# Kernel optimization log

Hardware: AMD Instinct MI355X
Metric: run time of the kernel (lower is better)

The kernel has to match this reference:

```python
import jax, jax.numpy as jnp
import numpy as np

N_NODES = 100000
IN_CH = 128
HID = 64
N_EDGES = 1600000
NEG_SLOPE = 0.2


def setup_inputs() -> dict:
    key = jax.random.key(0)
    k1, k2, k3, k4, k5, k6 = jax.random.split(key, 6)
    x = jax.random.normal(k1, (N_NODES, IN_CH), dtype=jnp.float32)
    edge_index = jax.random.randint(k2, (2, N_EDGES), 0, N_NODES, dtype=jnp.int64)
    # Glorot-style init for GATConv params (heads=1)
    s_w = (2.0 / (IN_CH + HID)) ** 0.5
    W = jax.random.normal(k3, (IN_CH, HID), dtype=jnp.float32) * s_w
    s_a = (2.0 / (1 + HID)) ** 0.5
    att_src = jax.random.normal(k4, (HID,), dtype=jnp.float32) * s_a
    att_dst = jax.random.normal(k5, (HID,), dtype=jnp.float32) * s_a
    bias = jnp.zeros((HID,), dtype=jnp.float32)
    return {"x": x, "edge_index": edge_index, "W": W, "att_src": att_src,
            "att_dst": att_dst, "bias": bias}


def reference(x, edge_index, W, att_src, att_dst, bias):
    N = x.shape[0]
    # PyG GATConv default: add self-loops
    loop = jnp.arange(N, dtype=edge_index.dtype)
    src = jnp.concatenate([edge_index[0], loop])  # message source j
    dst = jnp.concatenate([edge_index[1], loop])  # message target i

    h = x @ W                      # [N, HID]
    a_src = h @ att_src            # [N]
    a_dst = h @ att_dst            # [N]

    # per-edge attention logit: LeakyReLU(a_src[j] + a_dst[i])
    e = jax.nn.leaky_relu(a_src[src] + a_dst[dst], NEG_SLOPE)  # [E+N]
    # numerically-stable segment softmax over destination node
    m = jax.ops.segment_max(e, dst, num_segments=N)
    e = jnp.exp(e - m[dst])
    denom = jax.ops.segment_sum(e, dst, num_segments=N)
    alpha = e / (denom[dst] + 1e-16)               # [E+N]

    # scatter-aggregate weighted source features, then bias
    out = jax.ops.segment_sum(alpha[:, None] * h[src], dst, num_segments=N)
    out = out + bias               # [N, HID]
    return out, alpha[:, None]     # alpha shaped [E+N, heads=1]
```

## Files before the change

kernel.cpp:

```cpp
#include <hip/hip_runtime.h>

#define NN 100000
#define IC 128
#define HD 64
#define NEG 0.2f
#define NPB 64
#define NBKT ((NN + NPB - 1) / NPB)
#define CAP 1536
#define TILE 4096
#define NIT 8

typedef float f32x4 __attribute__((ext_vector_type(4)));
typedef short s16x8 __attribute__((ext_vector_type(8)));

__device__ __forceinline__ unsigned short f32_to_bf16u(float f) {
  union { float f; unsigned int i; } v;
  v.f = f;
  unsigned int b = v.i;
  b += 0x7FFFu + ((b >> 16) & 1u);
  return (unsigned short)(b >> 16);
}

__global__ __launch_bounds__(256) void k_gemm(const float* __restrict__ x,
                                              const float* __restrict__ W,
                                              const float* __restrict__ att_s,
                                              const float* __restrict__ att_d,
                                              unsigned short* __restrict__ hb,
                                              float* __restrict__ as_,
                                              float* __restrict__ ad_,
                                              int* __restrict__ bktcur) {
  __shared__ unsigned short xb[64 * 128];
  __shared__ unsigned short wt[64 * 128];
  const int tid = threadIdx.x;
  const int n0 = blockIdx.x * 64;
  if (tid == 0 && blockIdx.x < NBKT) bktcur[blockIdx.x] = 0;

  #pragma unroll
  for (int i = 0; i < 8; ++i) {
    int f = i * 256 + tid;
    int r = f >> 5, k0 = (f & 31) << 2;
    float4 v = make_float4(0.f, 0.f, 0.f, 0.f);
    if (n0 + r < NN) v = *(const float4*)&x[(size_t)(n0 + r) * IC + k0];
    ushort4 u;
    u.x = f32_to_bf16u(v.x); u.y = f32_to_bf16u(v.y);
    u.z = f32_to_bf16u(v.z); u.w = f32_to_bf16u(v.w);
    int idx = r * 128 + k0;
    *(ushort4*)&xb[idx ^ ((r & 7) << 3)] = u;
  }
  #pragma unroll
  for (int i = 0; i < 8; ++i) {
    int f = i * 256 + tid;
    int k = f >> 4, c0 = (f & 15) << 2;
    float4 v = *(const float4*)&W[k * HD + c0];
    const float* vf = (const float*)&v;
    #pragma unroll
    for (int j = 0; j < 4; ++j) {
      int c = c0 + j;
      int idx = c * 128 + k;
      wt[idx ^ ((c & 7) << 3)] = f32_to_bf16u(vf[j]);
    }
  }
  __syncthreads();

  const int wv = tid >> 6, lane = tid & 63;
  const int fr = lane & 15;
  const int fq = lane >> 4;
  const int nodeR = wv * 16 + fr;
  f32x4 acc[4] = {};
  #pragma unroll
  for (int kb = 0; kb < 4; ++kb) {
    int ks = kb * 32 + fq * 8;
    int ia = nodeR * 128 + ks;
    s16x8 af = *(s16x8*)&xb[ia ^ ((nodeR & 7) << 3)];
    #pragma unroll
    for (int cg = 0; cg < 4; ++cg) {
      int col = cg * 16 + fr;
      int ib = col * 128 + ks;
      s16x8 bfr = *(s16x8*)&wt[ib ^ ((col & 7) << 3)];
      acc[cg] = __builtin_amdgcn_mfma_f32_16x16x32_bf16(af, bfr, acc[cg], 0, 0, 0);
    }
  }

  float atts[4], attd[4];
  #pragma unroll
  for (int cg = 0; cg < 4; ++cg) {
    atts[cg] = att_s[cg * 16 + fr];
    attd[cg] = att_d[cg * 16 + fr];
  }
  __syncthreads();
  unsigned short* ho = xb;

  #pragma unroll
  for (int j = 0; j < 4; ++j) {
    int nrel = wv * 16 + fq * 4 + j;
    float ps = acc[0][j]*atts[0] + acc[1][j]*atts[1]
             + acc[2][j]*atts[2] + acc[3][j]*atts[3];
    float pd = acc[0][j]*attd[0] + acc[1][j]*attd[1]
             + acc[2][j]*attd[2] + acc[3][j]*attd[3];
    #pragma unroll
    for (int mk = 1; mk < 16; mk <<= 1) {
      ps += __shfl_xor(ps, mk);
      pd += __shfl_xor(pd, mk);
    }
    if (fr == 0 && n0 + nrel < NN) { as_[n0 + nrel] = ps; ad_[n0 + nrel] = pd; }
    #pragma unroll
    for (int cg = 0; cg < 4; ++cg)
      ho[nrel * 72 + cg * 16 + fr] = f32_to_bf16u(acc[cg][j]);
  }
  __syncthreads();

  {
    int node = tid >> 2, ch = (tid & 3) << 4;
    if (n0 + node < NN) {
      ushort4 a0 = *(ushort4*)&ho[node * 72 + ch];
      ushort4 a1 = *(ushort4*)&ho[node * 72 + ch + 4];
      ushort4 a2 = *(ushort4*)&ho[node * 72 + ch + 8];
      ushort4 a3 = *(ushort4*)&ho[node * 72 + ch + 12];
      unsigned short* dst = &hb[(size_t)(n0 + node) * HD + ch];
      *(ushort4*)(dst) = a0;
      *(ushort4*)(dst + 4) = a1;
      *(ushort4*)(dst + 8) = a2;
      *(ushort4*)(dst + 12) = a3;
    }
  }
}

__global__ __launch_bounds__(512) void k_part(const int* __restrict__ ei,
                                              const float* __restrict__ as_,
                                              const float* __restrict__ ad_,
                                              int* __restrict__ bktcur,
                                              int2* __restrict__ bktbuf,
                                              float* __restrict__ p_lin,
                                              int E, int M) {
  __shared__ int lcnt[NBKT];
  __shared__ int gbs[NBKT];
  const int tid = threadIdx.x;
  const int base = blockIdx.x * TILE;

  for (int c = tid; c < NBKT; c += 512) lcnt[c] = 0;
  __syncthreads();

  int pkx[NIT], rb[NIT];
  float tv[NIT];
  #pragma unroll
  for (int i = 0; i < NIT; ++i) {
    int m = base + i * 512 + tid;
    if (m < M) {
      int s, d;
      if (m < E) { s = ei[m]; d = ei[E + m]; }
      else       { s = m - E; d = s; }
      int b = d >> 6;
      pkx[i] = (s << 6) | (d & 63);
      tv[i] = as_[s] + ad_[d];
      int r = atomicAdd(&lcnt[b], 1);
      rb[i] = (b << 12) | r;
    } else rb[i] = -1;
  }
  __syncthreads();

  for (int c = tid; c < NBKT; c += 512) {
    int v = lcnt[c];
    gbs[c] = v ? atomicAdd(&bktcur[c], v) : 0;
  }
  __syncthreads();

  #pragma unroll
  for (int i = 0; i < NIT; ++i) {
    if (rb[i] >= 0) {
      int m = base + i * 512 + tid;
      float t = tv[i];
      t = t > 0.f ? t : NEG * t;
      float p = __expf(t);
      p_lin[m] = p;
      int b = (unsigned)rb[i] >> 12, r = rb[i] & 4095;
      int slot = gbs[b] + r;
      if (slot < CAP)
        bktbuf[(size_t)b * CAP + slot] = make_int2(pkx[i], __float_as_int(p));
    }
  }
}

__global__ __launch_bounds__(256) void k_pg(const int* __restrict__ bktcur,
                                            const int2* __restrict__ bktbuf,
                                            const unsigned short* __restrict__ hb,
                                            const float* __restrict__ bias,
                                            float* __restrict__ out,
                                            float* __restrict__ denom) {
  __shared__ int2 sp[CAP];
  __shared__ int cnt2[NPB], nstart[NPB], cur[NPB];
  __shared__ float dls[NPB];
  const int b = blockIdx.x;
  const int d0 = b << 6;
  const int tid = threadIdx.x;
  const int cnt = min(bktcur[b], CAP);
  const int2* mybuf = bktbuf + (size_t)b * CAP;
  const char* hbb = (const char*)hb;

  if (tid < NPB) { cnt2[tid] = 0; dls[tid] = 0.f; }
  __syncthreads();
  for (int e = tid; e < cnt; e += 256) atomicAdd(&cnt2[mybuf[e].x & 63], 1);
  __syncthreads();

  if (tid < 64) {
    int a = cnt2[tid];
    int va = a;
    #pragma unroll
    for (int off = 1; off < 64; off <<= 1) {
      int na = __shfl_up(va, off);
      if (tid >= off) va += na;
    }
    nstart[tid] = va - a;
    cur[tid] = va - a;
  }
  __syncthreads();
  for (int e = tid; e < cnt; e += 256) {
    int2 v = mybuf[e];
    int slot = atomicAdd(&cur[v.x & 63], 1);
    sp[slot] = make_int2((v.x & ~63) << 1, v.y);
  }
  __syncthreads();

  const int wv = tid >> 6, lane = tid & 63;
  const int half = lane >> 5;
  const int hl = lane & 31;
  const unsigned chb = (unsigned)hl << 2;
  const float2 bs2 = *(const float2*)&bias[2 * hl];

  for (int n = wv; n < NPB; n += 4) {
    if (d0 + n >= NN) break;
    int beg = nstart[n], end = beg + cnt2[n];
    float ax = 0.f, ay = 0.f, dens = 0.f;
    int e = beg;
    for (; e + 8 <= end; e += 8) {
      #pragma unroll
      for (int j = 0; j < 4; ++j) {
        int2 v = sp[e + 2 * j + half];
        unsigned u = *(const unsigned*)(hbb + ((unsigned)v.x + chb));
        float p = __int_as_float(v.y);
        dens += p;
        ax += p * __uint_as_float(u << 16);
        ay += p * __uint_as_float(u & 0xffff0000u);
      }
    }
    {
      #pragma unroll
      for (int j = 0; j < 4; ++j) {
        int idx = e + 2 * j + half;
        if (idx < end) {
          int2 v = sp[idx];
          unsigned u = *(const unsigned*)(hbb + ((unsigned)v.x + chb));
          float p = __int_as_float(v.y);
          dens += p;
          ax += p * __uint_as_float(u << 16);
          ay += p * __uint_as_float(u & 0xffff0000u);
        }
      }
    }
    ax += __shfl_xor(ax, 32);
    ay += __shfl_xor(ay, 32);
    dens += __shfl_xor(dens, 32);
    if (half == 0) {
      float rd = 1.f / (dens + 1e-16f);
      float2 o;
      o.x = ax * rd + bs2.x;
      o.y = ay * rd + bs2.y;
      *(float2*)&out[(size_t)(d0 + n) * HD + 2 * hl] = o;
      if (hl == 0) dls[n] = dens;
    }
  }
  __syncthreads();
  if (tid < NPB && d0 + tid < NN) denom[d0 + tid] = dls[tid];
}

__global__ __launch_bounds__(256) void k_alpha(const int* __restrict__ ei,
                                               const float* __restrict__ p_lin,
                                               const float* __restrict__ denom,
                                               float* __restrict__ alpha_out,
                                               int E, int M) {
  int m = blockIdx.x * 256 + threadIdx.x;
  if (m >= M) return;
  int d = (m < E) ? ei[E + m] : (m - E);
  alpha_out[m] = p_lin[m] / (denom[d] + 1e-16f);
}

extern "C" void kernel_launch(void* const* d_in, const int* in_sizes, int n_in,
                              void* d_out, int out_size, void* d_ws, size_t ws_size,
                              hipStream_t stream) {
  const float* x     = (const float*)d_in[0];
  const int*   ei    = (const int*)d_in[1];
  const float* W     = (const float*)d_in[2];
  const float* att_s = (const float*)d_in[3];
  const float* att_d = (const float*)d_in[4];
  const float* bias  = (const float*)d_in[5];

  const int E = in_sizes[1] / 2;
  const int M = E + NN;

  float* out       = (float*)d_out;
  float* alpha_out = out + (size_t)NN * HD;

  char* w = (char*)d_ws;
  auto alloc = [&](size_t bytes) {
    char* p = w;
    w += (bytes + 15) & ~(size_t)15;
    return p;
  };
  unsigned short* hb = (unsigned short*)alloc(sizeof(unsigned short) * (size_t)NN * HD);
  float* as_    = (float*)alloc(sizeof(float) * NN);
  float* ad_    = (float*)alloc(sizeof(float) * NN);
  float* denom  = (float*)alloc(sizeof(float) * NN);
  float* p_lin  = (float*)alloc(sizeof(float) * (size_t)M);
  int*   bktcur = (int*)alloc(sizeof(int) * NBKT);
  int2*  bktbuf = (int2*)alloc(sizeof(int2) * (size_t)NBKT * CAP);

  k_gemm<<<(NN + 63) / 64, 256, 0, stream>>>(x, W, att_s, att_d, hb, as_, ad_,
                                             bktcur);
  k_part<<<(M + TILE - 1) / TILE, 512, 0, stream>>>(ei, as_, ad_, bktcur,
                                                    bktbuf, p_lin, E, M);
  k_pg<<<NBKT, 256, 0, stream>>>(bktcur, bktbuf, hb, bias, out, denom);
  k_alpha<<<(M + 255) / 256, 256, 0, stream>>>(ei, p_lin, denom, alpha_out,
                                               E, M);
}
```

Measured before the change: 105.8 us.

## Split destination-bucket counters into 8 partitions to cut global atomic contention

The partition kernel now writes each edge into one of 8 per-partition bucket arrays (chosen by block index), so global atomicAdds on bucket cursors spread over 8x more counters. The gather kernel loads all partition segments of its bucket into shared memory before the per-node sort, which adds an extra LDS staging pass and doubles shared memory use (two CAP-sized int2 arrays). Per-partition capacity of 256 could overflow for skewed inputs and silently drop edges.

```diff
diff --git a/kernel.cpp b/kernel.cpp
--- a/kernel.cpp
+++ b/kernel.cpp
@@ -7,6 +7,8 @@
 #define NPB 64
 #define NBKT ((NN + NPB - 1) / NPB)
 #define CAP 1536
+#define CAP2 256
+#define NPART 8
 #define TILE 4096
 #define NIT 8
 
@@ -33,7 +35,7 @@
   __shared__ unsigned short wt[64 * 128];
   const int tid = threadIdx.x;
   const int n0 = blockIdx.x * 64;
-  if (tid == 0 && blockIdx.x < NBKT) bktcur[blockIdx.x] = 0;
+  if (tid < NPART && blockIdx.x < NBKT) bktcur[tid * NBKT + blockIdx.x] = 0;
 
   #pragma unroll
   for (int i = 0; i < 8; ++i) {
@@ -136,6 +138,9 @@
   __shared__ int gbs[NBKT];
   const int tid = threadIdx.x;
   const int base = blockIdx.x * TILE;
+  const int part = blockIdx.x & (NPART - 1);
+  int* mycur = bktcur + part * NBKT;
+  int2* mybuf = bktbuf + (size_t)part * NBKT * CAP2;
 
   for (int c = tid; c < NBKT; c += 512) lcnt[c] = 0;
   __syncthreads();
@@ -160,7 +165,7 @@
 
   for (int c = tid; c < NBKT; c += 512) {
     int v = lcnt[c];
-    gbs[c] = v ? atomicAdd(&bktcur[c], v) : 0;
+    gbs[c] = v ? atomicAdd(&mycur[c], v) : 0;
   }
   __syncthreads();
 
@@ -174,8 +179,8 @@
       p_lin[m] = p;
       int b = (unsigned)rb[i] >> 12, r = rb[i] & 4095;
       int slot = gbs[b] + r;
-      if (slot < CAP)
-        bktbuf[(size_t)b * CAP + slot] = make_int2(pkx[i], __float_as_int(p));
+      if (slot < CAP2)
+        mybuf[(size_t)b * CAP2 + slot] = make_int2(pkx[i], __float_as_int(p));
     }
   }
 }
@@ -186,19 +191,36 @@
                                             const float* __restrict__ bias,
                                             float* __restrict__ out,
                                             float* __restrict__ denom) {
+  __shared__ int2 spRaw[CAP];
   __shared__ int2 sp[CAP];
   __shared__ int cnt2[NPB], nstart[NPB], cur[NPB];
   __shared__ float dls[NPB];
+  __shared__ int pcnt[NPART], pbase[NPART];
   const int b = blockIdx.x;
   const int d0 = b << 6;
   const int tid = threadIdx.x;
-  const int cnt = min(bktcur[b], CAP);
-  const int2* mybuf = bktbuf + (size_t)b * CAP;
   const char* hbb = (const char*)hb;
 
   if (tid < NPB) { cnt2[tid] = 0; dls[tid] = 0.f; }
-  __syncthreads();
-  for (int e = tid; e < cnt; e += 256) atomicAdd(&cnt2[mybuf[e].x & 63], 1);
+  if (tid < NPART) pcnt[tid] = min(bktcur[tid * NBKT + b], CAP2);
+  __syncthreads();
+  if (tid == 0) {
+    int s = 0;
+    #pragma unroll
+    for (int p = 0; p < NPART; ++p) { pbase[p] = s; s += pcnt[p]; }
+  }
+  __syncthreads();
+  const int total = min(pbase[NPART - 1] + pcnt[NPART - 1], CAP);
+
+  for (int p = 0; p < NPART; ++p) {
+    const int2* src = bktbuf + ((size_t)p * NBKT + b) * CAP2;
+    int pb = pbase[p], pc = pcnt[p];
+    for (int e = tid; e < pc; e += 256)
+      if (pb + e < CAP) spRaw[pb + e] = src[e];
+  }
+  __syncthreads();
+
+  for (int e = tid; e < total; e += 256) atomicAdd(&cnt2[spRaw[e].x & 63], 1);
   __syncthreads();
 
   if (tid < 64) {
@@ -213,10 +235,10 @@
     cur[tid] = va - a;
   }
   __syncthreads();
-  for (int e = tid; e < cnt; e += 256) {
-    int2 v = mybuf[e];
+  for (int e = tid; e < total; e += 256) {
+    int2 v = spRaw[e];
     int slot = atomicAdd(&cur[v.x & 63], 1);
-    sp[slot] = make_int2((v.x & ~63) << 1, v.y);
+    if (slot < CAP) sp[slot] = make_int2((v.x & ~63) << 1, v.y);
   }
   __syncthreads();
 
@@ -228,7 +250,7 @@
 
   for (int n = wv; n < NPB; n += 4) {
     if (d0 + n >= NN) break;
-    int beg = nstart[n], end = beg + cnt2[n];
+    int beg = nstart[n], end = min(beg + cnt2[n], CAP);
     float ax = 0.f, ay = 0.f, dens = 0.f;
     int e = beg;
     for (; e + 8 <= end; e += 8) {
@@ -310,8 +332,8 @@
   float* ad_    = (float*)alloc(sizeof(float) * NN);
   float* denom  = (float*)alloc(sizeof(float) * NN);
   float* p_lin  = (float*)alloc(sizeof(float) * (size_t)M);
-  int*   bktcur = (int*)alloc(sizeof(int) * NBKT);
-  int2*  bktbuf = (int2*)alloc(sizeof(int2) * (size_t)NBKT * CAP);
+  int*   bktcur = (int*)alloc(sizeof(int) * NPART * NBKT);
+  int2*  bktbuf = (int2*)alloc(sizeof(int2) * (size_t)NPART * NBKT * CAP2);
 
   k_gemm<<<(NN + 63) / 64, 256, 0, stream>>>(x, W, att_s, att_d, hb, as_, ad_,
                                              bktcur);
```

Result: slower. 130.4 us (+23.2%).
